# Kernel tuning notes

Hardware: AMD Instinct MI355X
Metric: run time of the kernel (lower is better)

The kernel has to match this reference:

```python
import jax, jax.numpy as jnp
import numpy as np

B, DIN, DP, DOUT, K, N = 4, 64, 3, 64, 16, 8192


def setup_inputs() -> dict:
    key = jax.random.key(0)
    ks = jax.random.split(key, 5)
    features = jax.random.normal(ks[0], (B, DIN, N), dtype=jnp.float32)
    positions = jax.random.normal(ks[1], (B, DP, N), dtype=jnp.float32)
    neighborhoods = jax.random.randint(ks[2], (B, K, N), 0, N, dtype=jnp.int32)
    position_theta = jax.random.normal(ks[3], (DP, DIN, DOUT), dtype=jnp.float32) * 0.05
    position_bias = jnp.zeros((DIN, DOUT), dtype=jnp.float32)
    feature_bias = jnp.zeros((DOUT, 1), dtype=jnp.float32)
    return {
        "features": features,
        "positions": positions,
        "neighborhoods": neighborhoods,
        "position_theta": position_theta,
        "position_bias": position_bias,
        "feature_bias": feature_bias,
    }


def _gather_neighbors(x, idx):
    # x: [D, N], idx: [K, N] -> [D, K, N]
    return x[:, idx]


def reference(features, positions, neighborhoods, position_theta, position_bias, feature_bias):
    # Gather neighbor features/positions: [B, D, K, N]
    fg = jax.vmap(_gather_neighbors)(features, neighborhoods)      # [B, Din, K, N]
    pg = jax.vmap(_gather_neighbors)(positions, neighborhoods)     # [B, Dp,  K, N]
    # Relative positions of neighbors w.r.t. center point
    rel = pg - positions[:, :, None, :]                            # [B, Dp, K, N]
    # Dynamic weight w[b,k,n] = theta . rel + bias, contracted with
    # gathered features and summed over K, without materializing [Din,Dout] per neighbor.
    y = jnp.einsum('pio,bpkn,bikn->bon', position_theta, rel, fg)
    y = y + jnp.einsum('io,bikn->bon', position_bias, fg)
    # feature bias [Dout, 1] broadcasts over [B, Dout, N]
    y = y + feature_bias[None, :, :]
    return y  # [B, Dout, N]; activation=None (linear)
```

## Files before the change

kernel.cpp:

```cpp
#include <hip/hip_runtime.h>

#define NB    4
#define DIN_  64
#define DOUT_ 64
#define KN    16
#define NPT   8192
#define CPAD  264

typedef __attribute__((ext_vector_type(8))) short short8;
typedef __attribute__((ext_vector_type(4))) float v4f;

__device__ __forceinline__ float bf2f(unsigned short u) {
    unsigned int x = ((unsigned int)u) << 16;
    float f; __builtin_memcpy(&f, &x, 4); return f;
}
__device__ __forceinline__ unsigned short f2bf(float f) {
    unsigned int x; __builtin_memcpy(&x, &f, 4);
    x += 0x7fffu + ((x >> 16) & 1u);
    return (unsigned short)(x >> 16);
}

__global__ void k_prep(const float* __restrict__ feat, const float* __restrict__ pos,
                       const float* __restrict__ theta, const float* __restrict__ pbias,
                       unsigned short* __restrict__ ft, float4* __restrict__ pt,
                       unsigned short* __restrict__ tbs) {
    __shared__ float tile[64][65];
    const int bid = blockIdx.x;
    if (bid < 512) {
        int b = bid >> 7, n0 = (bid & 127) << 6;
        int lane = threadIdx.x & 63, w = threadIdx.x >> 6;
#pragma unroll
        for (int r = 0; r < 16; ++r) {
            int i = (r << 2) | w;
            tile[i][lane] = feat[(b*DIN_ + i)*NPT + n0 + lane];
        }
        __syncthreads();
#pragma unroll
        for (int r = 0; r < 16; ++r) {
            int n = (r << 2) | w;
            ft[((size_t)(b*NPT + n0 + n))*DIN_ + lane] = f2bf(tile[lane][n]);
        }
    } else if (bid < 640) {
        int t = (bid - 512)*256 + threadIdx.x;
        int b = t >> 13, n = t & 8191;
        float4 v;
        v.x = pos[(b*3 + 0)*NPT + n];
        v.y = pos[(b*3 + 1)*NPT + n];
        v.z = pos[(b*3 + 2)*NPT + n];
        v.w = 1.0f;
        pt[t] = v;
    } else {
        int e = (bid - 640)*256 + threadIdx.x;
        int w  = e >> 9;
        int ks = (e >> 6) & 7;
        int ln = e & 63;
        int orow = (w << 4) + (ln & 15);
        int koff = (ks << 5) + ((ln >> 4) << 3);
        short8 u;
#pragma unroll
        for (int j = 0; j < 8; ++j) {
            int c = koff + j;
            float v = (c < 192) ? theta[c*64 + orow] : pbias[(c - 192)*64 + orow];
            u[j] = (short)f2bf(v);
        }
        *reinterpret_cast<short8*>(tbs + (size_t)e*8) = u;
    }
}

template<bool USE_WS>
__global__ __launch_bounds__(256, 4) void k_main(
    const float*          __restrict__ feat,
    const float*          __restrict__ pos,
    const int*            __restrict__ nbr,
    const float*          __restrict__ theta,
    const float*          __restrict__ pbias,
    const float*          __restrict__ fbias,
    const unsigned short* __restrict__ ft,
    const float4*         __restrict__ pt,
    const unsigned short* __restrict__ tbs,
    float*                __restrict__ out)
{
    __shared__ __align__(16) unsigned short Xt[32*CPAD];
    __shared__ int    nbs[KN*32];
    __shared__ float4 pcs[32];
    __shared__ float4 ptk[32][16];
    __shared__ __align__(16) float out_s[64][32];

    const int tid  = threadIdx.x;
    const int lane = tid & 63;
    const int w    = tid >> 6;
    const int j16  = lane & 15;
    const int pt2  = lane >> 4;

    const int base = blockIdx.x << 5;
    const int b    = base >> 13;
    const int nb0  = base & 8191;

#pragma unroll
    for (int r = 0; r < 2; ++r) {
        int idx = tid + (r << 8);
        int k = idx >> 5, c = idx & 31;
        nbs[idx] = nbr[(b*KN + k)*NPT + nb0 + c];
    }
    if (tid < 128) {
        if (USE_WS) {
            ((float*)pcs)[tid] = ((const float*)(pt + b*NPT + nb0))[tid];
        } else if (tid < 32) {
            int n = nb0 + tid;
            pcs[tid] = make_float4(pos[(b*3+0)*NPT + n], pos[(b*3+1)*NPT + n],
                                   pos[(b*3+2)*NPT + n], 1.0f);
        }
    }
    __syncthreads();

    const unsigned short* ftb = ft + (((size_t)b) << 19);
    const float4*         ptb = pt + b*NPT;

#pragma unroll
    for (int pass = 0; pass < 2; ++pass) {
        const int q = (w << 3) + (pass << 2) + pt2;
        const float4 pc = pcs[q];

        float acc[4][4];
#pragma unroll
        for (int p = 0; p < 4; ++p)
#pragma unroll
            for (int j = 0; j < 4; ++j) acc[p][j] = 0.f;

        if (USE_WS) {
            const int idp = nbs[(j16 << 5) + q];
            ptk[q][j16] = ptb[idp];

            ushort4 frA[8], frB[8];
#pragma unroll
            for (int k = 0; k < 8; ++k) {
                const int id = nbs[(k << 5) + q];
                frA[k] = *reinterpret_cast<const ushort4*>(
                    ftb + (((size_t)id) << 6) + (j16 << 2));
            }
#pragma unroll
            for (int k = 0; k < 8; ++k) {
                const int id = nbs[((k + 8) << 5) + q];
                frB[k] = *reinterpret_cast<const ushort4*>(
                    ftb + (((size_t)id) << 6) + (j16 << 2));
            }
#pragma unroll
            for (int k = 0; k < 8; ++k) {
                const float4 pg = ptk[q][k];
                float f[4] = { bf2f(frA[k].x), bf2f(frA[k].y),
                               bf2f(frA[k].z), bf2f(frA[k].w) };
#pragma unroll
                for (int j = 0; j < 4; ++j) {
                    acc[0][j] += pg.x * f[j];
                    acc[1][j] += pg.y * f[j];
                    acc[2][j] += pg.z * f[j];
                    acc[3][j] += f[j];
                }
            }
#pragma unroll
            for (int k = 0; k < 8; ++k) {
                const float4 pg = ptk[q][k + 8];
                float f[4] = { bf2f(frB[k].x), bf2f(frB[k].y),
                               bf2f(frB[k].z), bf2f(frB[k].w) };
#pragma unroll
                for (int j = 0; j < 4; ++j) {
                    acc[0][j] += pg.x * f[j];
                    acc[1][j] += pg.y * f[j];
                    acc[2][j] += pg.z * f[j];
                    acc[3][j] += f[j];
                }
            }
        } else {
#pragma unroll 4
            for (int k = 0; k < KN; ++k) {
                const int id = nbs[(k << 5) + q];
                float4 pg; float f[4];
                pg.x = pos[(b*3+0)*NPT + id];
                pg.y = pos[(b*3+1)*NPT + id];
                pg.z = pos[(b*3+2)*NPT + id];
                pg.w = 1.0f;
#pragma unroll
                for (int j = 0; j < 4; ++j)
                    f[j] = feat[(b*DIN_ + (j16<<2) + j)*NPT + id];
#pragma unroll
                for (int j = 0; j < 4; ++j) {
                    acc[0][j] += pg.x * f[j];
                    acc[1][j] += pg.y * f[j];
                    acc[2][j] += pg.z * f[j];
                    acc[3][j] += f[j];
                }
            }
        }
#pragma unroll
        for (int j = 0; j < 4; ++j) {
            acc[0][j] -= pc.x * acc[3][j];
            acc[1][j] -= pc.y * acc[3][j];
            acc[2][j] -= pc.z * acc[3][j];
        }
#pragma unroll
        for (int p = 0; p < 4; ++p) {
            ushort4 pk;
            pk.x = f2bf(acc[p][0]); pk.y = f2bf(acc[p][1]);
            pk.z = f2bf(acc[p][2]); pk.w = f2bf(acc[p][3]);
            *reinterpret_cast<ushort4*>(&Xt[q*CPAD + (p<<6) + (j16<<2)]) = pk;
        }
    }
    __syncthreads();

    const int kg   = pt2;
    const int orow = (w << 4) + j16;
    v4f acc0 = {0.f,0.f,0.f,0.f}, acc1 = {0.f,0.f,0.f,0.f};
#pragma unroll
    for (int ks = 0; ks < 8; ++ks) {
        const int koff = (ks << 5) + (kg << 3);
        short8 a;
        if (USE_WS) {
            a = *reinterpret_cast<const short8*>(
                tbs + ((size_t)(((w << 3) + ks) << 6) + lane) * 8);
        } else {
#pragma unroll
            for (int j = 0; j < 8; ++j) {
                int c = koff + j;
                float v = (c < 192) ? theta[c*64 + orow] : pbias[(c - 192)*64 + orow];
                a[j] = (short)f2bf(v);
            }
        }
        short8 b0 = *reinterpret_cast<const short8*>(&Xt[j16*CPAD + koff]);
        short8 b1 = *reinterpret_cast<const short8*>(&Xt[(16 + j16)*CPAD + koff]);
        acc0 = __builtin_amdgcn_mfma_f32_16x16x32_bf16(a, b0, acc0, 0, 0, 0);
        acc1 = __builtin_amdgcn_mfma_f32_16x16x32_bf16(a, b1, acc1, 0, 0, 0);
    }
#pragma unroll
    for (int r = 0; r < 4; ++r) {
        const int o = (w << 4) + (kg << 2) + r;
        const float fb = fbias[o];
        out_s[o][j16]      = acc0[r] + fb;
        out_s[o][16 + j16] = acc1[r] + fb;
    }
    __syncthreads();
#pragma unroll
    for (int rep = 0; rep < 2; ++rep) {
        const int c  = tid + (rep << 8);
        const int o  = c >> 3, seg = c & 7;
        const float4 v = *reinterpret_cast<const float4*>(&out_s[o][seg << 2]);
        *reinterpret_cast<float4*>(
            &out[(size_t)(b*DOUT_ + o)*NPT + nb0 + (seg << 2)]) = v;
    }
}

extern "C" void kernel_launch(void* const* d_in, const int* in_sizes, int n_in,
                              void* d_out, int out_size, void* d_ws, size_t ws_size,
                              hipStream_t stream) {
    const float* feat  = (const float*)d_in[0];
    const float* pos   = (const float*)d_in[1];
    const int*   nbr   = (const int*)d_in[2];
    const float* theta = (const float*)d_in[3];
    const float* pbias = (const float*)d_in[4];
    const float* fbias = (const float*)d_in[5];
    float* out = (float*)d_out;

    const size_t ft_bytes  = (size_t)NB*NPT*DIN_*2;
    const size_t pt_bytes  = (size_t)NB*NPT*sizeof(float4);
    const size_t tbs_bytes = (size_t)DOUT_*256*2;
    const int n_blocks = (NB*NPT)/32;

    if (ws_size >= ft_bytes + pt_bytes + tbs_bytes) {
        unsigned short* ft  = (unsigned short*)d_ws;
        float4*         pt  = (float4*)((char*)d_ws + ft_bytes);
        unsigned short* tbs = (unsigned short*)((char*)d_ws + ft_bytes + pt_bytes);
        k_prep<<<648, 256, 0, stream>>>(feat, pos, theta, pbias, ft, pt, tbs);
        k_main<true><<<n_blocks, 256, 0, stream>>>(feat, pos, nbr, theta, pbias, fbias,
                                                   ft, pt, tbs, out);
    } else {
        k_main<false><<<n_blocks, 256, 0, stream>>>(feat, pos, nbr, theta, pbias, fbias,
                                                    (const unsigned short*)feat,
                                                    (const float4*)feat,
                                                    (const unsigned short*)feat, out);
    }
}
```

Before: 82.01 us.

## Remap blocks to XCDs per batch and prefetch sibling half into local L2

Block indices are remapped so that each of the 8 XCDs (blockIdx mod 8) handles a single batch and a single half of the points, in both the prep kernel and the main kernel. The aim is to keep each batch's gathered feature and position rows resident in that XCD's L2 rather than spread across all XCDs. Each main-kernel block also issues dummy loads of the matching slice from the other half of its batch, held live with an empty asm, to warm its L2 with data it will gather at random. This adds extra global reads per block, and the mapping assumes round-robin dispatch of blocks to XCDs.

```diff
diff --git a/kernel.cpp b/kernel.cpp
--- a/kernel.cpp
+++ b/kernel.cpp
@@ -27,7 +27,9 @@
     __shared__ float tile[64][65];
     const int bid = blockIdx.x;
     if (bid < 512) {
-        int b = bid >> 7, n0 = (bid & 127) << 6;
+        int xcd = bid & 7, cidx = bid >> 3;
+        int b = xcd & 3;
+        int n0 = (((xcd >> 2) << 6) + cidx) << 6;
         int lane = threadIdx.x & 63, w = threadIdx.x >> 6;
 #pragma unroll
         for (int r = 0; r < 16; ++r) {
@@ -41,14 +43,16 @@
             ft[((size_t)(b*NPT + n0 + n))*DIN_ + lane] = f2bf(tile[lane][n]);
         }
     } else if (bid < 640) {
-        int t = (bid - 512)*256 + threadIdx.x;
-        int b = t >> 13, n = t & 8191;
+        int pb  = bid - 512;
+        int xcd = pb & 7, idx = pb >> 3;
+        int b   = xcd & 3;
+        int n   = (((xcd >> 2) << 12) + (idx << 8)) + threadIdx.x;
         float4 v;
         v.x = pos[(b*3 + 0)*NPT + n];
         v.y = pos[(b*3 + 1)*NPT + n];
         v.z = pos[(b*3 + 2)*NPT + n];
         v.w = 1.0f;
-        pt[t] = v;
+        pt[b*NPT + n] = v;
     } else {
         int e = (bid - 640)*256 + threadIdx.x;
         int w  = e >> 9;
@@ -92,9 +96,24 @@
     const int j16  = lane & 15;
     const int pt2  = lane >> 4;
 
-    const int base = blockIdx.x << 5;
-    const int b    = base >> 13;
-    const int nb0  = base & 8191;
+    const int bid   = blockIdx.x;
+    const int xcd   = bid & 7;
+    const int cidx  = bid >> 3;
+    const int b     = xcd & 3;
+    const int half  = xcd >> 2;
+    const int nb0   = (((half << 7) + cidx) << 5) & 8191;
+
+    const unsigned short* ftb = ft + (((size_t)b) << 19);
+    const float4*         ptb = pt + b*NPT;
+
+    float4 s0 = make_float4(0.f,0.f,0.f,0.f), s1 = s0;
+    if (USE_WS) {
+        const int sib0 = (half ^ 1) << 12;
+        const float4* swf = reinterpret_cast<const float4*>(
+            ftb + ((size_t)(sib0 + (cidx << 5)) << 6));
+        s0 = swf[tid];
+        if (tid < 32) s1 = ptb[sib0 + (cidx << 5) + tid];
+    }
 
 #pragma unroll
     for (int r = 0; r < 2; ++r) {
@@ -104,17 +123,15 @@
     }
     if (tid < 128) {
         if (USE_WS) {
-            ((float*)pcs)[tid] = ((const float*)(pt + b*NPT + nb0))[tid];
+            ((float*)pcs)[tid] = ((const float*)(ptb + nb0))[tid];
         } else if (tid < 32) {
             int n = nb0 + tid;
             pcs[tid] = make_float4(pos[(b*3+0)*NPT + n], pos[(b*3+1)*NPT + n],
                                    pos[(b*3+2)*NPT + n], 1.0f);
         }
     }
+    asm volatile("" :: "v"(s0.x), "v"(s0.w), "v"(s1.x), "v"(s1.w));
     __syncthreads();
-
-    const unsigned short* ftb = ft + (((size_t)b) << 19);
-    const float4*         ptb = pt + b*NPT;
 
 #pragma unroll
     for (int pass = 0; pass < 2; ++pass) {
```

After: 86.61 us. 5.6% more time.
